# Kernel tuning notes

Hardware: AMD Instinct MI355X
Metric: run time of the kernel (lower is better)

## Reference

```python
import jax, jax.numpy as jnp
import numpy as np

N = 50000
E = 800000


def gcn_conv(x, W, b, src, dst, n_nodes):
    # PyG GCNConv: add self-loops, symmetric deg^-1/2 normalization,
    # out[dst] += norm * (x @ W)[src], then bias.
    h = x @ W  # [N, out]
    src_sl = jnp.concatenate([src, jnp.arange(n_nodes, dtype=src.dtype)])
    dst_sl = jnp.concatenate([dst, jnp.arange(n_nodes, dtype=dst.dtype)])
    deg = jax.ops.segment_sum(jnp.ones_like(dst_sl, dtype=h.dtype), dst_sl,
                              num_segments=n_nodes)  # in-degree incl. self-loop
    dinv = jnp.where(deg > 0, jax.lax.rsqrt(deg), 0.0)
    norm = dinv[src_sl] * dinv[dst_sl]  # [E+N]
    msg = norm[:, None] * h[src_sl]  # gather + scale, [E+N, out]
    out = jax.ops.segment_sum(msg, dst_sl, num_segments=n_nodes)
    return out + b


def setup_inputs() -> dict:
    key = jax.random.key(0)
    ks = jax.random.split(key, 8)
    F, H, O = 128, 128, 64
    x = jax.random.normal(ks[0], (N, F), dtype=jnp.float32)
    edge_index = jax.random.randint(ks[1], (2, E), 0, N, dtype=jnp.int64)
    # Glorot-ish scaled weights
    W1 = jax.random.normal(ks[2], (F, H), dtype=jnp.float32) / np.sqrt(F)
    b1 = jnp.zeros((H,), dtype=jnp.float32)
    W2 = jax.random.normal(ks[3], (H, H), dtype=jnp.float32) / np.sqrt(H)
    b2 = jnp.zeros((H,), dtype=jnp.float32)
    W3 = jax.random.normal(ks[4], (H, O), dtype=jnp.float32) / np.sqrt(H)
    b3 = jnp.zeros((O,), dtype=jnp.float32)
    return {"x": x, "edge_index": edge_index, "W1": W1, "b1": b1,
            "W2": W2, "b2": b2, "W3": W3, "b3": b3}


def reference(x, edge_index, W1, b1, W2, b2, W3, b3):
    src, dst = edge_index[0], edge_index[1]
    h = gcn_conv(x, W1, b1, src, dst, N)
    h = jax.nn.elu(h)
    h = gcn_conv(h, W2, b2, src, dst, N)
    h = jax.nn.elu(h)
    h = gcn_conv(h, W3, b3, src, dst, N)
    return h
```

## Files before the change

### kernel.cpp

```cpp
#include <hip/hip_runtime.h>
#include <hip/hip_fp16.h>
#include <math.h>


#define NFEAT_IN 128
#define SCAN_CHUNK 2048
#define NSHARD 8

typedef _Float16 f16x8 __attribute__((ext_vector_type(8)));
typedef float f32x4 __attribute__((ext_vector_type(4)));

__global__ void zero_kernel(int4* __restrict__ p, int n4, int4* __restrict__ eswpad) {
    int i = blockIdx.x * blockDim.x + threadIdx.x;
    int4 z; z.x = z.y = z.z = z.w = 0;
    if (i < n4) p[i] = z;
    if (i < 8) eswpad[i] = z;
}

__global__ __launch_bounds__(256) void count_kernel(const int* __restrict__ dst,
                                                    int* __restrict__ cnt,
                                                    int E, int shard_sz) {
    int shard = blockIdx.x & (NSHARD - 1);
    int blk = blockIdx.x >> 3;
    int nblk = gridDim.x >> 3;
    int lo = shard * shard_sz, hi = lo + shard_sz;
    int stride = nblk * blockDim.x;
    int E4 = E >> 2;
    for (int g = blk * blockDim.x + threadIdx.x; g < E4; g += stride) {
        int4 d = *(const int4*)&dst[g * 4];
        if (d.x >= lo && d.x < hi) atomicAdd(&cnt[d.x], 1);
        if (d.y >= lo && d.y < hi) atomicAdd(&cnt[d.y], 1);
        if (d.z >= lo && d.z < hi) atomicAdd(&cnt[d.z], 1);
        if (d.w >= lo && d.w < hi) atomicAdd(&cnt[d.w], 1);
    }
    if (blockIdx.x == 0 && threadIdx.x < (E & 3)) {
        int d = dst[(E & ~3) + threadIdx.x];
        atomicAdd(&cnt[d], 1);
    }
}

__global__ __launch_bounds__(256) void reduce_kernel(const int* __restrict__ cnt,
                                                     int* __restrict__ bsum, int n) {
    __shared__ int wtot[4];
    int b = blockIdx.x, t = threadIdx.x;
    int base = b * SCAN_CHUNK + t * 8;
    int s = 0;
    if (base + 8 <= n) {
        int4 a = *(const int4*)&cnt[base];
        int4 c = *(const int4*)&cnt[base + 4];
        s = a.x + a.y + a.z + a.w + c.x + c.y + c.z + c.w;
    } else {
        for (int i = 0; i < 8; ++i) if (base + i < n) s += cnt[base + i];
    }
    int lane = t & 63, wid = t >> 6;
    #pragma unroll
    for (int off = 32; off > 0; off >>= 1) s += __shfl_down(s, off, 64);
    if (lane == 0) wtot[wid] = s;
    __syncthreads();
    if (t == 0) bsum[b] = wtot[0] + wtot[1] + wtot[2] + wtot[3];
}

__global__ __launch_bounds__(256) void scan3_kernel(const int* __restrict__ cnt,
                                                    const int* __restrict__ bsum,
                                                    int* __restrict__ offs,
                                                    int* __restrict__ pos,
                                                    float* __restrict__ dinv,
                                                    int n, int nb) {
    __shared__ int wtot[4];
    __shared__ int sbase;
    int b = blockIdx.x, t = threadIdx.x;
    if (t < 64) {
        int val = (t < nb) ? bsum[t] : 0;
        int pre = (t < b) ? val : 0;
        int tot = val;
        #pragma unroll
        for (int off = 32; off > 0; off >>= 1) {
            pre += __shfl_down(pre, off, 64);
            tot += __shfl_down(tot, off, 64);
        }
        if (t == 0) {
            sbase = pre;
            if (b == nb - 1) offs[n] = tot;
        }
    }
    int base = b * SCAN_CHUNK + t * 8;
    int v[8];
    #pragma unroll
    for (int i = 0; i < 8; ++i) v[i] = (base + i < n) ? cnt[base + i] : 0;
    int psum[8], s = 0;
    #pragma unroll
    for (int i = 0; i < 8; ++i) { psum[i] = s; s += v[i]; }
    int lane = t & 63, wid = t >> 6;
    int inc = s;
    #pragma unroll
    for (int off = 1; off < 64; off <<= 1) {
        int tt = __shfl_up(inc, off, 64);
        if (lane >= off) inc += tt;
    }
    if (lane == 63) wtot[wid] = inc;
    __syncthreads();
    int wb = 0;
    for (int w = 0; w < wid; ++w) wb += wtot[w];
    int tbase = sbase + wb + (inc - s);
    #pragma unroll
    for (int i = 0; i < 8; ++i) {
        if (base + i < n) {
            int o = tbase + psum[i];
            offs[base + i] = o;
            pos[base + i] = o;
            dinv[base + i] = rsqrtf((float)(v[i] + 1));
        }
    }
}

__global__ __launch_bounds__(256) void fill_kernel(const int* __restrict__ src,
                                                   const int* __restrict__ dst,
                                                   int* __restrict__ pos,
                                                   const float* __restrict__ dinv,
                                                   int2* __restrict__ esw,
                                                   int E, int shard_sz) {
    int shard = blockIdx.x & (NSHARD - 1);
    int blk = blockIdx.x >> 3;
    int nblk = gridDim.x >> 3;
    int lo = shard * shard_sz;
    int hi = lo + shard_sz;
    int stride = nblk * blockDim.x;
    for (int i = blk * blockDim.x + threadIdx.x; i < E; i += stride) {
        int d = dst[i];
        if (d >= lo && d < hi) {
            int s = src[i];
            int p = atomicAdd(&pos[d], 1);
            float ds = dinv[s];
            __half2 w2 = __floats2half2_rn(ds, ds);
            int2 e;
            e.x = s;
            e.y = *(int*)&w2;
            esw[p] = e;
        }
    }
}

__global__ __launch_bounds__(256) void convx_kernel(const float* __restrict__ x,
                                                    f16x8* __restrict__ Xf, int nchunk) {
    int i = blockIdx.x * blockDim.x + threadIdx.x;
    if (i >= nchunk) return;
    int m = i >> 4, kc = i & 15;
    float4 a = *(const float4*)&x[(size_t)m * 128 + kc * 8];
    float4 b = *(const float4*)&x[(size_t)m * 128 + kc * 8 + 4];
    f16x8 v;
    v[0] = (_Float16)a.x; v[1] = (_Float16)a.y; v[2] = (_Float16)a.z; v[3] = (_Float16)a.w;
    v[4] = (_Float16)b.x; v[5] = (_Float16)b.y; v[6] = (_Float16)b.z; v[7] = (_Float16)b.w;
    int kt = kc >> 2, sub = kc & 3;
    Xf[(size_t)((m >> 4) * 4 + kt) * 64 + sub * 16 + (m & 15)] = v;
}

__global__ void wfrag_kernel(const float* __restrict__ W1, const float* __restrict__ W2,
                             const float* __restrict__ W3, f16x8* __restrict__ wf1,
                             f16x8* __restrict__ wf2, f16x8* __restrict__ wf3) {
    int b = blockIdx.x;
    const float* W; f16x8* Wf; int NT;
    if (b < 8)       { W = W1; Wf = wf1; NT = 8; }
    else if (b < 16) { W = W2; Wf = wf2; NT = 8; b -= 8; }
    else             { W = W3; Wf = wf3; NT = 4; b -= 16; }
    int c = b * 256 + threadIdx.x;
    if (c >= NT * 256) return;
    int BN = NT * 16;
    int nt = c >> 8;
    int kt = (c >> 6) & 3;
    int l = c & 63;
    int n = nt * 16 + (l & 15);
    int k0 = kt * 32 + (l >> 4) * 8;
    f16x8 v;
    #pragma unroll
    for (int j = 0; j < 8; ++j) v[j] = (_Float16)W[(size_t)(k0 + j) * BN + n];
    Wf[c] = v;
}

template <int NT>
__global__ __launch_bounds__(256) void mgemm_kernel(const f16x8* __restrict__ Xf,
                                                    const f16x8* __restrict__ Wg,
                                                    __half* __restrict__ Y, int mtiles) {
    constexpr int BN = NT * 16;
    __shared__ f16x8 Wf[NT * 4 * 64];
    int t = threadIdx.x;
    #pragma unroll
    for (int i = 0; i < NT; ++i) Wf[t + i * 256] = Wg[t + i * 256];
    __syncthreads();
    int lane = t & 63;
    int mt0 = blockIdx.x * 8 + (t >> 6) * 2;
    #pragma unroll
    for (int it = 0; it < 2; ++it) {
        int mtile = mt0 + it;
        if (mtile >= mtiles) continue;
        const f16x8* xb = Xf + (size_t)mtile * 4 * 64;
        f16x8 bf[4];
        #pragma unroll
        for (int kt = 0; kt < 4; ++kt) bf[kt] = xb[kt * 64 + lane];
        f32x4 acc[NT];
        #pragma unroll
        for (int nt = 0; nt < NT; ++nt) acc[nt] = (f32x4){0.f, 0.f, 0.f, 0.f};
        #pragma unroll
        for (int kt = 0; kt < 4; ++kt) {
            #pragma unroll
            for (int nt = 0; nt < NT; ++nt) {
                f16x8 af = Wf[(nt * 4 + kt) * 64 + lane];
                acc[nt] = __builtin_amdgcn_mfma_f32_16x16x32_f16(af, bf[kt], acc[nt], 0, 0, 0);
            }
        }
        int m = mtile * 16 + (lane & 15);
        int nc0 = (lane >> 4) * 4;
        #pragma unroll
        for (int nt = 0; nt < NT; ++nt) {
            union { __half2 h2[2]; uint2 u; } pk;
            pk.h2[0] = __floats2half2_rn(acc[nt][0], acc[nt][1]);
            pk.h2[1] = __floats2half2_rn(acc[nt][2], acc[nt][3]);
            *(uint2*)&Y[(size_t)m * BN + nt * 16 + nc0] = pk.u;
        }
    }
}

__global__ __launch_bounds__(256) void agg128_kernel(const __half* __restrict__ H,
                                                     const int* __restrict__ offs,
                                                     const int2* __restrict__ esw,
                                                     const float* __restrict__ dinv,
                                                     const float* __restrict__ bias,
                                                     uint4* __restrict__ outf, int n) {
    int lane = threadIdx.x & 63;
    int q = lane >> 4;
    int fl = lane & 15;
    int v = blockIdx.x * 4 + (threadIdx.x >> 6);
    if (v >= n) return;
    float dv = dinv[v];
    int e0 = offs[v], e1 = offs[v + 1];
    int cntE = e1 - e0;
    int nfull = cntE >> 4;
    const char* Hb = (const char*)H + fl * 16;
    __half2 acc[4];
    __half2 zh = __floats2half2_rn(0.f, 0.f);
    acc[0] = zh; acc[1] = zh; acc[2] = zh; acc[3] = zh;
    int e = e0 + q;
    for (int i = 0; i < nfull; ++i, e += 16) {
        #pragma unroll
        for (int j = 0; j < 4; ++j) {
            int2 p = esw[e + 4 * j];
            __half2 w2 = *(__half2*)&p.y;
            uint4 hq = *(const uint4*)(Hb + ((size_t)(unsigned)p.x << 8));
            const __half2* h2 = (const __half2*)&hq;
            acc[0] = __hfma2(h2[0], w2, acc[0]);
            acc[1] = __hfma2(h2[1], w2, acc[1]);
            acc[2] = __hfma2(h2[2], w2, acc[2]);
            acc[3] = __hfma2(h2[3], w2, acc[3]);
        }
    }
    if (cntE & 15) {
        #pragma unroll
        for (int j = 0; j < 4; ++j) {
            int ee = e + 4 * j;
            int2 p = esw[ee];
            int wi = (ee < e1) ? p.y : 0;
            __half2 w2 = *(__half2*)&wi;
            uint4 hq = *(const uint4*)(Hb + ((size_t)(unsigned)p.x << 8));
            const __half2* h2 = (const __half2*)&hq;
            acc[0] = __hfma2(h2[0], w2, acc[0]);
            acc[1] = __hfma2(h2[1], w2, acc[1]);
            acc[2] = __hfma2(h2[2], w2, acc[2]);
            acc[3] = __hfma2(h2[3], w2, acc[3]);
        }
    }
    #pragma unroll
    for (int m = 16; m <= 32; m <<= 1) {
        #pragma unroll
        for (int k = 0; k < 4; ++k) {
            int ai = *(int*)&acc[k];
            int bi = __shfl_xor(ai, m, 64);
            acc[k] = __hadd2(acc[k], *(__half2*)&bi);
        }
    }
    if (q == 0) {
        float a[8];
        #pragma unroll
        for (int k = 0; k < 4; ++k) {
            float2 f = __half22float2(acc[k]);
            a[2 * k] = f.x; a[2 * k + 1] = f.y;
        }
        uint4 hq = *(const uint4*)(Hb + ((size_t)(unsigned)v << 8));
        const _Float16* hp = (const _Float16*)&hq;
        float b[8];
        *(float4*)&b[0] = *(const float4*)&bias[fl * 8];
        *(float4*)&b[4] = *(const float4*)&bias[fl * 8 + 4];
        float r[8];
        #pragma unroll
        for (int k = 0; k < 8; ++k) {
            float t2 = fmaf((float)hp[k], dv, a[k]);
            r[k] = fmaf(dv, t2, b[k]);
            r[k] = r[k] > 0.f ? r[k] : (__expf(r[k]) - 1.f);
        }
        union { __half2 h2[4]; uint4 u; } pk;
        pk.h2[0] = __floats2half2_rn(r[0], r[1]);
        pk.h2[1] = __floats2half2_rn(r[2], r[3]);
        pk.h2[2] = __floats2half2_rn(r[4], r[5]);
        pk.h2[3] = __floats2half2_rn(r[6], r[7]);
        int blockc = (v >> 4) * 4 + (fl >> 2);
        int l2 = (fl & 3) * 16 + (v & 15);
        outf[(size_t)blockc * 64 + l2] = pk.u;
    }
}

__global__ __launch_bounds__(256) void agg64_kernel(const __half* __restrict__ H,
                                                    const int* __restrict__ offs,
                                                    const int2* __restrict__ esw,
                                                    const float* __restrict__ dinv,
                                                    const float* __restrict__ bias,
                                                    float* __restrict__ out, int n) {
    int lane = threadIdx.x & 63;
    int q = lane >> 3;
    int fl = lane & 7;
    int v = blockIdx.x * 4 + (threadIdx.x >> 6);
    if (v >= n) return;
    float dv = dinv[v];
    int e0 = offs[v], e1 = offs[v + 1];
    int cntE = e1 - e0;
    int nfull = cntE >> 4;
    const char* Hb = (const char*)H + fl * 16;
    float a[8];
    #pragma unroll
    for (int k = 0; k < 8; ++k) a[k] = 0.f;
    int e = e0 + q;
    for (int i = 0; i < nfull; ++i, e += 16) {
        #pragma unroll
        for (int j = 0; j < 2; ++j) {
            int2 p = esw[e + 8 * j];
            float w = __low2float(*(const __half2*)&p.y);
            uint4 hq = *(const uint4*)(Hb + ((size_t)(unsigned)p.x << 7));
            const _Float16* hp = (const _Float16*)&hq;
            #pragma unroll
            for (int k = 0; k < 8; ++k) a[k] = fmaf((float)hp[k], w, a[k]);
        }
    }
    if (cntE & 15) {
        #pragma unroll
        for (int j = 0; j < 2; ++j) {
            int ee = e + 8 * j;
            int2 p = esw[ee];
            float w = (ee < e1) ? __low2float(*(const __half2*)&p.y) : 0.f;
            uint4 hq = *(const uint4*)(Hb + ((size_t)(unsigned)p.x << 7));
            const _Float16* hp = (const _Float16*)&hq;
            #pragma unroll
            for (int k = 0; k < 8; ++k) a[k] = fmaf((float)hp[k], w, a[k]);
        }
    }
    #pragma unroll
    for (int m = 8; m <= 32; m <<= 1) {
        #pragma unroll
        for (int k = 0; k < 8; ++k) a[k] += __shfl_xor(a[k], m, 64);
    }
    if (q == 0) {
        uint4 hq = *(const uint4*)(Hb + ((size_t)(unsigned)v << 7));
        const _Float16* hp = (const _Float16*)&hq;
        float b[8];
        *(float4*)&b[0] = *(const float4*)&bias[fl * 8];
        *(float4*)&b[4] = *(const float4*)&bias[fl * 8 + 4];
        float r[8];
        #pragma unroll
        for (int k = 0; k < 8; ++k) {
            float t2 = fmaf((float)hp[k], dv, a[k]);
            r[k] = fmaf(dv, t2, b[k]);
        }
        float4 o0, o1;
        o0.x = r[0]; o0.y = r[1]; o0.z = r[2]; o0.w = r[3];
        o1.x = r[4]; o1.y = r[5]; o1.z = r[6]; o1.w = r[7];
        *(float4*)&out[(size_t)v * 64 + fl * 8] = o0;
        *(float4*)&out[(size_t)v * 64 + fl * 8 + 4] = o1;
    }
}

static inline size_t alignup(size_t x) { return (x + 255) & ~(size_t)255; }

extern "C" void kernel_launch(void* const* d_in, const int* in_sizes, int n_in,
                              void* d_out, int out_size, void* d_ws, size_t ws_size,
                              hipStream_t stream) {
    const float* x  = (const float*)d_in[0];
    const int*   ei = (const int*)d_in[1];
    const float* W1 = (const float*)d_in[2];
    const float* b1 = (const float*)d_in[3];
    const float* W2 = (const float*)d_in[4];
    const float* b2 = (const float*)d_in[5];
    const float* W3 = (const float*)d_in[6];
    const float* b3 = (const float*)d_in[7];
    float* out = (float*)d_out;

    const int N = in_sizes[0] / NFEAT_IN;
    const int E = in_sizes[1] / 2;
    const int* src = ei;
    const int* dst = ei + E;

    char* w = (char*)d_ws;
    int* cnt  = (int*)w;  w += alignup((size_t)N * sizeof(int));
    int* pos  = (int*)w;  w += alignup((size_t)N * sizeof(int));
    int* offs = (int*)w;  w += alignup((size_t)(N + 1) * sizeof(int));
    float* dinv = (float*)w; w += alignup((size_t)N * sizeof(float));
    int* bsum = (int*)w;  w += alignup((size_t)64 * sizeof(int));
    int2* esw = (int2*)w; w += alignup((size_t)(E + 16) * sizeof(int2));
    __half* fA = (__half*)w; w += alignup((size_t)N * 128 * sizeof(__half));
    __half* hB = (__half*)w; w += alignup((size_t)N * 128 * sizeof(__half));
    f16x8* wf1 = (f16x8*)w; w += alignup((size_t)2048 * sizeof(f16x8));
    f16x8* wf2 = (f16x8*)w; w += alignup((size_t)2048 * sizeof(f16x8));
    f16x8* wf3 = (f16x8*)w; w += alignup((size_t)1024 * sizeof(f16x8));

    const int nb = (N + SCAN_CHUNK - 1) / SCAN_CHUNK;
    const int shard_sz = (N + NSHARD - 1) / NSHARD;
    const int mtiles = N / 16;

    zero_kernel<<<(N / 4 + 255) / 256, 256, 0, stream>>>((int4*)cnt, N / 4, (int4*)(esw + E));
    count_kernel<<<NSHARD * 128, 256, 0, stream>>>(dst, cnt, E, shard_sz);
    reduce_kernel<<<nb, 256, 0, stream>>>(cnt, bsum, N);
    scan3_kernel<<<nb, 256, 0, stream>>>(cnt, bsum, offs, pos, dinv, N, nb);
    fill_kernel<<<NSHARD * 128, 256, 0, stream>>>(src, dst, pos, dinv, esw, E, shard_sz);

    wfrag_kernel<<<20, 256, 0, stream>>>(W1, W2, W3, wf1, wf2, wf3);
    convx_kernel<<<(N * 16 + 255) / 256, 256, 0, stream>>>(x, (f16x8*)fA, N * 16);

    int gemm_grid = (mtiles + 7) / 8;
    int agg_grid = (N + 3) / 4;

    mgemm_kernel<8><<<gemm_grid, 256, 0, stream>>>((const f16x8*)fA, wf1, hB, mtiles);
    agg128_kernel<<<agg_grid, 256, 0, stream>>>(hB, offs, esw, dinv, b1, (uint4*)fA, N);
    mgemm_kernel<8><<<gemm_grid, 256, 0, stream>>>((const f16x8*)fA, wf2, hB, mtiles);
    agg128_kernel<<<agg_grid, 256, 0, stream>>>(hB, offs, esw, dinv, b2, (uint4*)fA, N);
    mgemm_kernel<4><<<gemm_grid, 256, 0, stream>>>((const f16x8*)fA, wf3, hB, mtiles);
    agg64_kernel<<<agg_grid, 256, 0, stream>>>(hB, offs, esw, dinv, b3, out, N);
}
```

Before: 220.4 us.

## Build CSR with per-edge atomic ranks instead of sharded count and fill passes

The count kernel now records each edge's atomicAdd return value as its rank within its destination bucket, and the fill kernel computes the slot as offs[dst]+rank without any atomics. This removes the 8-way sharded rescans of the edge list in both count and fill, along with the second round of atomics on pos. In exchange it stores an E-sized rank array, and the count kernel's atomics now run over all destinations at once instead of one shard at a time, which may reduce locality. Edge order within a bucket stays nondeterministic.

```diff
diff --git a/kernel.cpp b/kernel.cpp
--- a/kernel.cpp
+++ b/kernel.cpp
@@ -5,7 +5,6 @@
 
 #define NFEAT_IN 128
 #define SCAN_CHUNK 2048
-#define NSHARD 8
 
 typedef _Float16 f16x8 __attribute__((ext_vector_type(8)));
 typedef float f32x4 __attribute__((ext_vector_type(4)));
@@ -17,25 +16,21 @@
     if (i < 8) eswpad[i] = z;
 }
 
-__global__ __launch_bounds__(256) void count_kernel(const int* __restrict__ dst,
-                                                    int* __restrict__ cnt,
-                                                    int E, int shard_sz) {
-    int shard = blockIdx.x & (NSHARD - 1);
-    int blk = blockIdx.x >> 3;
-    int nblk = gridDim.x >> 3;
-    int lo = shard * shard_sz, hi = lo + shard_sz;
-    int stride = nblk * blockDim.x;
-    int E4 = E >> 2;
-    for (int g = blk * blockDim.x + threadIdx.x; g < E4; g += stride) {
-        int4 d = *(const int4*)&dst[g * 4];
-        if (d.x >= lo && d.x < hi) atomicAdd(&cnt[d.x], 1);
-        if (d.y >= lo && d.y < hi) atomicAdd(&cnt[d.y], 1);
-        if (d.z >= lo && d.z < hi) atomicAdd(&cnt[d.z], 1);
-        if (d.w >= lo && d.w < hi) atomicAdd(&cnt[d.w], 1);
-    }
-    if (blockIdx.x == 0 && threadIdx.x < (E & 3)) {
-        int d = dst[(E & ~3) + threadIdx.x];
-        atomicAdd(&cnt[d], 1);
+__global__ __launch_bounds__(256) void countrank_kernel(const int* __restrict__ dst,
+                                                        int* __restrict__ cnt,
+                                                        int* __restrict__ rank, int E) {
+    int i = blockIdx.x * blockDim.x + threadIdx.x;
+    int base = i * 4;
+    if (base + 4 <= E) {
+        int4 d = *(const int4*)&dst[base];
+        int4 r;
+        r.x = atomicAdd(&cnt[d.x], 1);
+        r.y = atomicAdd(&cnt[d.y], 1);
+        r.z = atomicAdd(&cnt[d.z], 1);
+        r.w = atomicAdd(&cnt[d.w], 1);
+        *(int4*)&rank[base] = r;
+    } else {
+        for (int k = base; k < E; ++k) rank[k] = atomicAdd(&cnt[dst[k]], 1);
     }
 }
 
@@ -63,7 +58,6 @@
 __global__ __launch_bounds__(256) void scan3_kernel(const int* __restrict__ cnt,
                                                     const int* __restrict__ bsum,
                                                     int* __restrict__ offs,
-                                                    int* __restrict__ pos,
                                                     float* __restrict__ dinv,
                                                     int n, int nb) {
     __shared__ int wtot[4];
@@ -105,36 +99,46 @@
     #pragma unroll
     for (int i = 0; i < 8; ++i) {
         if (base + i < n) {
-            int o = tbase + psum[i];
-            offs[base + i] = o;
-            pos[base + i] = o;
+            offs[base + i] = tbase + psum[i];
             dinv[base + i] = rsqrtf((float)(v[i] + 1));
         }
     }
 }
 
-__global__ __launch_bounds__(256) void fill_kernel(const int* __restrict__ src,
-                                                   const int* __restrict__ dst,
-                                                   int* __restrict__ pos,
-                                                   const float* __restrict__ dinv,
-                                                   int2* __restrict__ esw,
-                                                   int E, int shard_sz) {
-    int shard = blockIdx.x & (NSHARD - 1);
-    int blk = blockIdx.x >> 3;
-    int nblk = gridDim.x >> 3;
-    int lo = shard * shard_sz;
-    int hi = lo + shard_sz;
-    int stride = nblk * blockDim.x;
-    for (int i = blk * blockDim.x + threadIdx.x; i < E; i += stride) {
-        int d = dst[i];
-        if (d >= lo && d < hi) {
-            int s = src[i];
-            int p = atomicAdd(&pos[d], 1);
-            float ds = dinv[s];
-            __half2 w2 = __floats2half2_rn(ds, ds);
-            int2 e;
-            e.x = s;
-            e.y = *(int*)&w2;
+__global__ __launch_bounds__(256) void fillr_kernel(const int* __restrict__ src,
+                                                    const int* __restrict__ dst,
+                                                    const int* __restrict__ rank,
+                                                    const int* __restrict__ offs,
+                                                    const float* __restrict__ dinv,
+                                                    int2* __restrict__ esw, int E) {
+    int i = blockIdx.x * blockDim.x + threadIdx.x;
+    int base = i * 4;
+    if (base + 4 <= E) {
+        int4 d = *(const int4*)&dst[base];
+        int4 r = *(const int4*)&rank[base];
+        int4 s = *(const int4*)&src[base];
+        int p0 = offs[d.x] + r.x;
+        int p1 = offs[d.y] + r.y;
+        int p2 = offs[d.z] + r.z;
+        int p3 = offs[d.w] + r.w;
+        float w0 = dinv[s.x], w1 = dinv[s.y], w2 = dinv[s.z], w3 = dinv[s.w];
+        __half2 h0 = __floats2half2_rn(w0, w0);
+        __half2 h1 = __floats2half2_rn(w1, w1);
+        __half2 h2 = __floats2half2_rn(w2, w2);
+        __half2 h3 = __floats2half2_rn(w3, w3);
+        int2 e0; e0.x = s.x; e0.y = *(int*)&h0;
+        int2 e1; e1.x = s.y; e1.y = *(int*)&h1;
+        int2 e2; e2.x = s.z; e2.y = *(int*)&h2;
+        int2 e3; e3.x = s.w; e3.y = *(int*)&h3;
+        esw[p0] = e0; esw[p1] = e1; esw[p2] = e2; esw[p3] = e3;
+    } else {
+        for (int k = base; k < E; ++k) {
+            int d = dst[k];
+            int p = offs[d] + rank[k];
+            int s = src[k];
+            float w = dinv[s];
+            __half2 h = __floats2half2_rn(w, w);
+            int2 e; e.x = s; e.y = *(int*)&h;
             esw[p] = e;
         }
     }
@@ -396,7 +400,7 @@
 
     char* w = (char*)d_ws;
     int* cnt  = (int*)w;  w += alignup((size_t)N * sizeof(int));
-    int* pos  = (int*)w;  w += alignup((size_t)N * sizeof(int));
+    int* rank = (int*)w;  w += alignup((size_t)E * sizeof(int));
     int* offs = (int*)w;  w += alignup((size_t)(N + 1) * sizeof(int));
     float* dinv = (float*)w; w += alignup((size_t)N * sizeof(float));
     int* bsum = (int*)w;  w += alignup((size_t)64 * sizeof(int));
@@ -408,14 +412,14 @@
     f16x8* wf3 = (f16x8*)w; w += alignup((size_t)1024 * sizeof(f16x8));
 
     const int nb = (N + SCAN_CHUNK - 1) / SCAN_CHUNK;
-    const int shard_sz = (N + NSHARD - 1) / NSHARD;
     const int mtiles = N / 16;
+    const int egrid = (E / 4 + 255) / 256;
 
     zero_kernel<<<(N / 4 + 255) / 256, 256, 0, stream>>>((int4*)cnt, N / 4, (int4*)(esw + E));
-    count_kernel<<<NSHARD * 128, 256, 0, stream>>>(dst, cnt, E, shard_sz);
+    countrank_kernel<<<egrid, 256, 0, stream>>>(dst, cnt, rank, E);
     reduce_kernel<<<nb, 256, 0, stream>>>(cnt, bsum, N);
-    scan3_kernel<<<nb, 256, 0, stream>>>(cnt, bsum, offs, pos, dinv, N, nb);
-    fill_kernel<<<NSHARD * 128, 256, 0, stream>>>(src, dst, pos, dinv, esw, E, shard_sz);
+    scan3_kernel<<<nb, 256, 0, stream>>>(cnt, bsum, offs, dinv, N, nb);
+    fillr_kernel<<<egrid, 256, 0, stream>>>(src, dst, rank, offs, dinv, esw, E);
 
     wfrag_kernel<<<20, 256, 0, stream>>>(W1, W2, W3, wf1, wf2, wf3);
     convx_kernel<<<(N * 16 + 255) / 256, 256, 0, stream>>>(x, (f16x8*)fA, N * 16);
```

After: 195.6 us. -11.3%, faster.
